# Performance work log

Measured on AMD Instinct MI355X. Metric: run time of the kernel, lower is better.

Reference implementation:

```python
import jax, jax.numpy as jnp
import numpy as np

# bitsandbytes NF4 codebook (16 levels, normalized to [-1, 1])
NF4_CODE = jnp.array([
    -1.0, -0.6961928009986877, -0.5250730514526367, -0.39491748809814453,
    -0.28444138169288635, -0.18477343022823334, -0.09105003625154495, 0.0,
    0.07958029955625534, 0.16093020141124725, 0.24611230194568634,
    0.33791524171829224, 0.44070982933044434, 0.5626170039176941,
    0.7229568362236023, 1.0], dtype=jnp.float32)

BLOCK = 64  # bitsandbytes default quantization blocksize
TOK, DIN, DOUT, RANK = 8192, 4096, 4096, 16
LORA_ALPHA = 16
SCALING = LORA_ALPHA / RANK ** 0.5  # rslora


def setup_inputs() -> dict:
    key = jax.random.key(0)
    k1, k2, k3, k4, k5, k6 = jax.random.split(key, 6)
    x = jax.random.normal(k1, (TOK, DIN), dtype=jnp.float32)
    w_codes = jax.random.randint(k2, (DOUT, DIN), 0, 16, dtype=jnp.int32)
    absmax = jax.random.uniform(k3, (DOUT, DIN // BLOCK), dtype=jnp.float32)
    bias = jax.random.normal(k4, (DOUT,), dtype=jnp.float32)
    lora_A = jax.random.normal(k5, (DIN, RANK), dtype=jnp.float32) * (1.0 / DIN ** 0.5)
    lora_B = jax.random.normal(k6, (RANK, DOUT), dtype=jnp.float32) * 0.02
    return {"x": x, "w_codes": w_codes, "absmax": absmax, "bias": bias,
            "lora_A": lora_A, "lora_B": lora_B}


def reference(x, w_codes, absmax, bias, lora_A, lora_B):
    # Dequantize NF4 base weight: codebook lookup * per-block absmax scale
    # W: [DOUT, DIN], absmax broadcast over blocks of 64 along DIN
    W = NF4_CODE[w_codes] * jnp.repeat(absmax, BLOCK, axis=1)
    base_out = x @ W.T + bias                      # [TOK, DOUT]
    lora_out = (x @ lora_A) @ lora_B               # low-rank path [TOK, DOUT]
    return base_out + lora_out * SCALING
```

## Files before the change

### kernel.cpp

```cpp
#include <hip/hip_runtime.h>
#include <hip/hip_bf16.h>
#include <cstdint>
#include <cstddef>

#define TOK   8192
#define DIN   4096
#define DOUT  4096
#define RANK  16
#define KE    4160
#define NKT64 (KE / 64)

#define BM 256
#define BN 256

#define PXB 512
#define DQB 8192
#define TLB 16

typedef __attribute__((ext_vector_type(8))) short bf16x8;
typedef __attribute__((ext_vector_type(4))) float f32x4;
typedef __attribute__((ext_vector_type(8))) unsigned short u16x8;

__device__ __constant__ float NF4_CODE_D[16] = {
    -1.0f, -0.6961928009986877f, -0.5250730514526367f, -0.39491748809814453f,
    -0.28444138169288635f, -0.18477343022823334f, -0.09105003625154495f, 0.0f,
    0.07958029955625534f, 0.16093020141124725f, 0.24611230194568634f,
    0.33791524171829224f, 0.44070982933044434f, 0.5626170039176941f,
    0.7229568362236023f, 1.0f};

__device__ __forceinline__ unsigned short f2bf(float f) {
    union { float f; unsigned u; } v; v.f = f;
    unsigned u = v.u;
    unsigned r = (u + 0x7FFFu + ((u >> 16) & 1u)) >> 16;
    return (unsigned short)r;
}

__device__ __forceinline__ void async_copy16(const void* g, void* l) {
    __builtin_amdgcn_global_load_lds(
        (const __attribute__((address_space(1))) void*)g,
        (__attribute__((address_space(3))) void*)l,
        16, 0, 0);
}

__global__ __launch_bounds__(256) void prep_fused(
        const float* __restrict__ x, const float* __restrict__ lora_A,
        const int* __restrict__ codes, const float* __restrict__ absmax,
        const float* __restrict__ bias, const float* __restrict__ lora_B,
        unsigned short* __restrict__ xe, unsigned short* __restrict__ we) {
    __shared__ float tab[16];
    const int bid = blockIdx.x;
    const int tid = threadIdx.x;

    if (bid < PXB) {
        const int l = tid & 63;
        const int w = tid >> 6;
        const int t0 = bid * 16 + w * 4;

        float p[4][16];
#pragma unroll
        for (int a = 0; a < 4; ++a)
#pragma unroll
            for (int r = 0; r < 16; ++r) p[a][r] = 0.f;

        for (int it = 0; it < 16; ++it) {
            const int kb = it * 256 + l * 4;
            float4 xv[4];
#pragma unroll
            for (int a = 0; a < 4; ++a)
                xv[a] = *(const float4*)(x + (size_t)(t0 + a) * DIN + kb);
#pragma unroll
            for (int a = 0; a < 4; ++a) {
                ushort4 s;
                s.x = f2bf(xv[a].x); s.y = f2bf(xv[a].y);
                s.z = f2bf(xv[a].z); s.w = f2bf(xv[a].w);
                *(ushort4*)(xe + (size_t)(t0 + a) * KE + kb) = s;
            }
#pragma unroll
            for (int j = 0; j < 4; ++j) {
                const float4* ap = (const float4*)(lora_A + (size_t)(kb + j) * RANK);
                const float4 a0 = ap[0], a1 = ap[1], a2 = ap[2], a3 = ap[3];
                const float av[16] = {a0.x, a0.y, a0.z, a0.w, a1.x, a1.y, a1.z, a1.w,
                                      a2.x, a2.y, a2.z, a2.w, a3.x, a3.y, a3.z, a3.w};
#pragma unroll
                for (int a = 0; a < 4; ++a) {
                    const float xs = (j == 0) ? xv[a].x : (j == 1) ? xv[a].y
                                    : (j == 2) ? xv[a].z : xv[a].w;
#pragma unroll
                    for (int r = 0; r < 16; ++r) p[a][r] += xs * av[r];
                }
            }
        }

#pragma unroll
        for (int a = 0; a < 4; ++a) {
#pragma unroll
            for (int r = 0; r < 16; ++r) {
                float v = p[a][r];
#pragma unroll
                for (int off = 32; off > 0; off >>= 1) v += __shfl_xor(v, off, 64);
                if (l == r)
                    xe[(size_t)(t0 + a) * KE + DIN + r] = f2bf(4.0f * v);
            }
            if (l >= 16)
                xe[(size_t)(t0 + a) * KE + DIN + l] =
                    (l == 16) ? (unsigned short)0x3F80u : (unsigned short)0u;
        }
    } else if (bid < PXB + DQB) {
        if (tid < 16) tab[tid] = NF4_CODE_D[tid];
        __syncthreads();
        const size_t t = (size_t)(bid - PXB) * 256 + tid;
        const size_t base = t * 8;
        const int o = (int)(base >> 12);
        const int k = (int)(base & (DIN - 1));
        const float am = absmax[base >> 6];
        const int4 c0 = *(const int4*)(codes + base);
        const int4 c1 = *(const int4*)(codes + base + 4);
        u16x8 ov;
        ov[0] = f2bf(tab[c0.x] * am);
        ov[1] = f2bf(tab[c0.y] * am);
        ov[2] = f2bf(tab[c0.z] * am);
        ov[3] = f2bf(tab[c0.w] * am);
        ov[4] = f2bf(tab[c1.x] * am);
        ov[5] = f2bf(tab[c1.y] * am);
        ov[6] = f2bf(tab[c1.z] * am);
        ov[7] = f2bf(tab[c1.w] * am);
        *(u16x8*)(we + (size_t)o * KE + k) = ov;
    } else {
        const int o = (bid - PXB - DQB) * 256 + tid;
        unsigned short* dst = we + (size_t)o * KE + DIN;
#pragma unroll
        for (int r = 0; r < RANK; ++r) dst[r] = f2bf(lora_B[(size_t)r * DOUT + o]);
        dst[16] = f2bf(bias[o]);
#pragma unroll
        for (int r = 17; r < 64; ++r) dst[r] = 0;
    }
}

__global__ __launch_bounds__(512, 2) void gemm_bt(const unsigned short* __restrict__ A,
                                                  const unsigned short* __restrict__ B,
                                                  float* __restrict__ C) {
    __shared__ __attribute__((aligned(1024))) char smem[4 * 32768];

    const int tid = threadIdx.x;
    const int l = tid & 63;
    const int w = tid >> 6;
    const int wm = w >> 2;
    const int wn = w & 3;

    const int tm = blockIdx.x >> 4;
    const int tn = blockIdx.x & 15;
    const int rowBase = tm * BM;
    const int colBase = tn * BN;

    int srow[2], scolb[2], loffs[2];
#pragma unroll
    for (int g = 0; g < 2; ++g) {
        const int loff = g * 8192 + tid * 16;
        const int soff = loff ^ (((loff >> 7) & 7) << 4);
        loffs[g] = loff;
        srow[g] = soff >> 6;
        scolb[g] = soff & 63;
    }

    auto stageA = [&](int tt, int kh, int slot) {
        char* dst = smem + slot * 32768;
        const int k0 = tt * 64 + kh * 32;
#pragma unroll
        for (int g = 0; g < 2; ++g)
            async_copy16((const char*)A + ((size_t)(rowBase + srow[g]) * KE + k0) * 2 + scolb[g],
                         dst + loffs[g]);
    };
    auto stageB = [&](int tt, int kh, int slot) {
        char* dst = smem + slot * 32768 + 16384;
        const int k0 = tt * 64 + kh * 32;
#pragma unroll
        for (int g = 0; g < 2; ++g)
            async_copy16((const char*)B + ((size_t)(colBase + srow[g]) * KE + k0) * 2 + scolb[g],
                         dst + loffs[g]);
    };

    const int lmask = ((l >> 1) & 7) << 4;
    const int aoff = (((wm * 128 + (l & 15)) * 64) + ((l >> 4) * 16)) ^ lmask;
    const int boff = (((wn * 64 + (l & 15)) * 64) + ((l >> 4) * 16)) ^ lmask;

    f32x4 acc[8][4];
#pragma unroll
    for (int m = 0; m < 8; ++m)
#pragma unroll
        for (int n = 0; n < 4; ++n) acc[m][n] = (f32x4){0.f, 0.f, 0.f, 0.f};

    bf16x8 aLo[4], aHi[4], aLo2[4], aHi2[4], bCur[4], bNxt[4];

    stageA(0, 0, 0); stageB(0, 0, 0);
    stageA(0, 1, 1); stageB(0, 1, 1);
    asm volatile("s_waitcnt vmcnt(4)" ::: "memory");
    __builtin_amdgcn_s_barrier();
    {
        const char* S0 = smem;
#pragma unroll
        for (int n = 0; n < 4; ++n)
            bCur[n] = *(const bf16x8*)(S0 + 16384 + boff + n * 1024);
#pragma unroll
        for (int m = 0; m < 4; ++m)
            aLo[m] = *(const bf16x8*)(S0 + aoff + m * 1024);
    }

    for (int t = 0; t < NKT64; ++t) {
        const char* S0 = smem + ((2 * t) & 3) * 32768;
        const char* S1 = smem + ((2 * t + 1) & 3) * 32768;
        const char* Sn = smem + ((2 * t + 2) & 3) * 32768;
        const int d0 = (2 * t + 2) & 3, d1 = (2 * t + 3) & 3;
        const bool more = (t + 1 < NKT64);

#pragma unroll
        for (int m = 0; m < 4; ++m)
            aHi[m] = *(const bf16x8*)(S0 + aoff + (4 + m) * 1024);
        if (more) { stageA(t + 1, 0, d0); stageB(t + 1, 0, d0); }
        __builtin_amdgcn_sched_barrier(0);
        __builtin_amdgcn_s_setprio(1);
#pragma unroll
        for (int m = 0; m < 4; ++m)
#pragma unroll
            for (int n = 0; n < 4; ++n)
                acc[m][n] = __builtin_amdgcn_mfma_f32_16x16x32_bf16(
                    aLo[m], bCur[n], acc[m][n], 0, 0, 0);
        __builtin_amdgcn_s_setprio(0);
        __builtin_amdgcn_sched_barrier(0);

        if (more) {
            asm volatile("s_waitcnt vmcnt(4)" ::: "memory");
        } else {
            asm volatile("s_waitcnt vmcnt(0)" ::: "memory");
        }
        __builtin_amdgcn_s_barrier();
        __builtin_amdgcn_sched_barrier(0);
#pragma unroll
        for (int n = 0; n < 4; ++n)
            bNxt[n] = *(const bf16x8*)(S1 + 16384 + boff + n * 1024);
#pragma unroll
        for (int m = 0; m < 4; ++m)
            aLo2[m] = *(const bf16x8*)(S1 + aoff + m * 1024);
        __builtin_amdgcn_sched_barrier(0);
        __builtin_amdgcn_s_setprio(1);
#pragma unroll
        for (int m = 0; m < 4; ++m)
#pragma unroll
            for (int n = 0; n < 4; ++n)
                acc[4 + m][n] = __builtin_amdgcn_mfma_f32_16x16x32_bf16(
                    aHi[m], bCur[n], acc[4 + m][n], 0, 0, 0);
        __builtin_amdgcn_s_setprio(0);
        __builtin_amdgcn_sched_barrier(0);

#pragma unroll
        for (int m = 0; m < 4; ++m)
            aHi2[m] = *(const bf16x8*)(S1 + aoff + (4 + m) * 1024);
        if (more) { stageA(t + 1, 1, d1); stageB(t + 1, 1, d1); }
        __builtin_amdgcn_sched_barrier(0);
        __builtin_amdgcn_s_setprio(1);
#pragma unroll
        for (int m = 0; m < 4; ++m)
#pragma unroll
            for (int n = 0; n < 4; ++n)
                acc[m][n] = __builtin_amdgcn_mfma_f32_16x16x32_bf16(
                    aLo2[m], bNxt[n], acc[m][n], 0, 0, 0);
        __builtin_amdgcn_s_setprio(0);
        __builtin_amdgcn_sched_barrier(0);

        if (more) {
            asm volatile("s_waitcnt vmcnt(4)" ::: "memory");
            __builtin_amdgcn_s_barrier();
            __builtin_amdgcn_sched_barrier(0);
#pragma unroll
            for (int n = 0; n < 4; ++n)
                bCur[n] = *(const bf16x8*)(Sn + 16384 + boff + n * 1024);
#pragma unroll
            for (int m = 0; m < 4; ++m)
                aLo[m] = *(const bf16x8*)(Sn + aoff + m * 1024);
        }
        __builtin_amdgcn_sched_barrier(0);
        __builtin_amdgcn_s_setprio(1);
#pragma unroll
        for (int m = 0; m < 4; ++m)
#pragma unroll
            for (int n = 0; n < 4; ++n)
                acc[4 + m][n] = __builtin_amdgcn_mfma_f32_16x16x32_bf16(
                    aHi2[m], bNxt[n], acc[4 + m][n], 0, 0, 0);
        __builtin_amdgcn_s_setprio(0);
        __builtin_amdgcn_sched_barrier(0);
    }

#pragma unroll
    for (int m = 0; m < 8; ++m) {
        const int rowg = rowBase + wm * 128 + m * 16 + (l >> 4) * 4;
#pragma unroll
        for (int n = 0; n < 4; ++n) {
            const int colg = colBase + wn * 64 + n * 16 + (l & 15);
            float* cp = C + (size_t)rowg * DOUT + colg;
#pragma unroll
            for (int r = 0; r < 4; ++r) cp[(size_t)r * DOUT] = acc[m][n][r];
        }
    }
}

extern "C" void kernel_launch(void* const* d_in, const int* in_sizes, int n_in,
                              void* d_out, int out_size, void* d_ws, size_t ws_size,
                              hipStream_t stream) {
    const float* x      = (const float*)d_in[0];
    const int*   codes  = (const int*)d_in[1];
    const float* absmax = (const float*)d_in[2];
    const float* bias   = (const float*)d_in[3];
    const float* lora_A = (const float*)d_in[4];
    const float* lora_B = (const float*)d_in[5];
    float* out = (float*)d_out;

    unsigned short* xe = (unsigned short*)d_ws;
    unsigned short* we = xe + (size_t)TOK * KE;

    prep_fused<<<PXB + DQB + TLB, 256, 0, stream>>>(x, lora_A, codes, absmax,
                                                    bias, lora_B, xe, we);
    gemm_bt<<<(TOK / BM) * (DOUT / BN), 512, 0, stream>>>(xe, we, out);
}
```

Baseline: 356.0 us.

## Switch GEMM to 32x32x16 MFMA, swizzle block order, and interleave A/B staging

Replaces the 16x16x32 bf16 MFMA tiles with 32x32x16 MFMA tiles. This changes the per-wave fragment layout, the LDS read offsets and the output store mapping. It also remaps blockIdx with a swizzle so that consecutive blocks share tiles for better L2 reuse. The A and B async loads are split and spread across phases, with the vmcnt waits adjusted to match. The larger MFMA shape reduces LDS fragment reads per FLOP, at the cost of a more complex schedule and a risk of mis-tuned wait counts.

```diff
diff --git a/kernel.cpp b/kernel.cpp
--- a/kernel.cpp
+++ b/kernel.cpp
@@ -18,7 +18,7 @@
 #define TLB 16
 
 typedef __attribute__((ext_vector_type(8))) short bf16x8;
-typedef __attribute__((ext_vector_type(4))) float f32x4;
+typedef __attribute__((ext_vector_type(16))) float f32x16;
 typedef __attribute__((ext_vector_type(8))) unsigned short u16x8;
 
 __device__ __constant__ float NF4_CODE_D[16] = {
@@ -147,8 +147,9 @@
     const int wm = w >> 2;
     const int wn = w & 3;
 
-    const int tm = blockIdx.x >> 4;
-    const int tn = blockIdx.x & 15;
+    const int swz = (blockIdx.x & 7) * 64 + (blockIdx.x >> 3);
+    const int tm = swz >> 4;
+    const int tn = swz & 15;
     const int rowBase = tm * BM;
     const int colBase = tn * BN;
 
@@ -179,15 +180,28 @@
                          dst + loffs[g]);
     };
 
+    const int r32 = l & 31;
+    const int h32 = (l >> 5) & 1;
     const int lmask = ((l >> 1) & 7) << 4;
-    const int aoff = (((wm * 128 + (l & 15)) * 64) + ((l >> 4) * 16)) ^ lmask;
-    const int boff = (((wn * 64 + (l & 15)) * 64) + ((l >> 4) * 16)) ^ lmask;
-
-    f32x4 acc[8][4];
-#pragma unroll
-    for (int m = 0; m < 8; ++m)
-#pragma unroll
-        for (int n = 0; n < 4; ++n) acc[m][n] = (f32x4){0.f, 0.f, 0.f, 0.f};
+    int aoffs[4][2], boffs[2][2];
+#pragma unroll
+    for (int mt = 0; mt < 4; ++mt)
+#pragma unroll
+        for (int kk = 0; kk < 2; ++kk)
+            aoffs[mt][kk] = (((wm * 128 + mt * 32 + r32) * 64) + kk * 32 + h32 * 16) ^ lmask;
+#pragma unroll
+    for (int nt = 0; nt < 2; ++nt)
+#pragma unroll
+        for (int kk = 0; kk < 2; ++kk)
+            boffs[nt][kk] = 16384 + ((((wn * 64 + nt * 32 + r32) * 64) + kk * 32 + h32 * 16) ^ lmask);
+
+    f32x16 acc[4][2];
+#pragma unroll
+    for (int mt = 0; mt < 4; ++mt)
+#pragma unroll
+        for (int nt = 0; nt < 2; ++nt)
+#pragma unroll
+            for (int r = 0; r < 16; ++r) acc[mt][nt][r] = 0.f;
 
     bf16x8 aLo[4], aHi[4], aLo2[4], aHi2[4], bCur[4], bNxt[4];
 
@@ -198,11 +212,15 @@
     {
         const char* S0 = smem;
 #pragma unroll
-        for (int n = 0; n < 4; ++n)
-            bCur[n] = *(const bf16x8*)(S0 + 16384 + boff + n * 1024);
-#pragma unroll
-        for (int m = 0; m < 4; ++m)
-            aLo[m] = *(const bf16x8*)(S0 + aoff + m * 1024);
+        for (int nt = 0; nt < 2; ++nt)
+#pragma unroll
+            for (int kk = 0; kk < 2; ++kk)
+                bCur[nt * 2 + kk] = *(const bf16x8*)(S0 + boffs[nt][kk]);
+#pragma unroll
+        for (int mt = 0; mt < 2; ++mt)
+#pragma unroll
+            for (int kk = 0; kk < 2; ++kk)
+                aLo[mt * 2 + kk] = *(const bf16x8*)(S0 + aoffs[mt][kk]);
     }
 
     for (int t = 0; t < NKT64; ++t) {
@@ -213,91 +231,115 @@
         const bool more = (t + 1 < NKT64);
 
 #pragma unroll
-        for (int m = 0; m < 4; ++m)
-            aHi[m] = *(const bf16x8*)(S0 + aoff + (4 + m) * 1024);
-        if (more) { stageA(t + 1, 0, d0); stageB(t + 1, 0, d0); }
+        for (int mt = 0; mt < 2; ++mt)
+#pragma unroll
+            for (int kk = 0; kk < 2; ++kk)
+                aHi[mt * 2 + kk] = *(const bf16x8*)(S0 + aoffs[2 + mt][kk]);
+        if (more) stageA(t + 1, 0, d0);
         __builtin_amdgcn_sched_barrier(0);
         __builtin_amdgcn_s_setprio(1);
 #pragma unroll
-        for (int m = 0; m < 4; ++m)
-#pragma unroll
-            for (int n = 0; n < 4; ++n)
-                acc[m][n] = __builtin_amdgcn_mfma_f32_16x16x32_bf16(
-                    aLo[m], bCur[n], acc[m][n], 0, 0, 0);
+        for (int kk = 0; kk < 2; ++kk)
+#pragma unroll
+            for (int mt = 0; mt < 2; ++mt)
+#pragma unroll
+                for (int nt = 0; nt < 2; ++nt)
+                    acc[mt][nt] = __builtin_amdgcn_mfma_f32_32x32x16_bf16(
+                        aLo[mt * 2 + kk], bCur[nt * 2 + kk], acc[mt][nt], 0, 0, 0);
         __builtin_amdgcn_s_setprio(0);
         __builtin_amdgcn_sched_barrier(0);
 
         if (more) {
-            asm volatile("s_waitcnt vmcnt(4)" ::: "memory");
+            asm volatile("s_waitcnt vmcnt(2)" ::: "memory");
         } else {
             asm volatile("s_waitcnt vmcnt(0)" ::: "memory");
         }
         __builtin_amdgcn_s_barrier();
         __builtin_amdgcn_sched_barrier(0);
 #pragma unroll
-        for (int n = 0; n < 4; ++n)
-            bNxt[n] = *(const bf16x8*)(S1 + 16384 + boff + n * 1024);
-#pragma unroll
-        for (int m = 0; m < 4; ++m)
-            aLo2[m] = *(const bf16x8*)(S1 + aoff + m * 1024);
+        for (int nt = 0; nt < 2; ++nt)
+#pragma unroll
+            for (int kk = 0; kk < 2; ++kk)
+                bNxt[nt * 2 + kk] = *(const bf16x8*)(S1 + boffs[nt][kk]);
+#pragma unroll
+        for (int mt = 0; mt < 2; ++mt)
+#pragma unroll
+            for (int kk = 0; kk < 2; ++kk)
+                aLo2[mt * 2 + kk] = *(const bf16x8*)(S1 + aoffs[mt][kk]);
+        if (more) stageB(t + 1, 0, d0);
         __builtin_amdgcn_sched_barrier(0);
         __builtin_amdgcn_s_setprio(1);
 #pragma unroll
-        for (int m = 0; m < 4; ++m)
-#pragma unroll
-            for (int n = 0; n < 4; ++n)
-                acc[4 + m][n] = __builtin_amdgcn_mfma_f32_16x16x32_bf16(
-                    aHi[m], bCur[n], acc[4 + m][n], 0, 0, 0);
+        for (int kk = 0; kk < 2; ++kk)
+#pragma unroll
+            for (int mt = 0; mt < 2; ++mt)
+#pragma unroll
+                for (int nt = 0; nt < 2; ++nt)
+                    acc[2 + mt][nt] = __builtin_amdgcn_mfma_f32_32x32x16_bf16(
+                        aHi[mt * 2 + kk], bCur[nt * 2 + kk], acc[2 + mt][nt], 0, 0, 0);
         __builtin_amdgcn_s_setprio(0);
         __builtin_amdgcn_sched_barrier(0);
 
 #pragma unroll
-        for (int m = 0; m < 4; ++m)
-            aHi2[m] = *(const bf16x8*)(S1 + aoff + (4 + m) * 1024);
-        if (more) { stageA(t + 1, 1, d1); stageB(t + 1, 1, d1); }
+        for (int mt = 0; mt < 2; ++mt)
+#pragma unroll
+            for (int kk = 0; kk < 2; ++kk)
+                aHi2[mt * 2 + kk] = *(const bf16x8*)(S1 + aoffs[2 + mt][kk]);
+        if (more) stageA(t + 1, 1, d1);
         __builtin_amdgcn_sched_barrier(0);
         __builtin_amdgcn_s_setprio(1);
 #pragma unroll
-        for (int m = 0; m < 4; ++m)
-#pragma unroll
-            for (int n = 0; n < 4; ++n)
-                acc[m][n] = __builtin_amdgcn_mfma_f32_16x16x32_bf16(
-                    aLo2[m], bNxt[n], acc[m][n], 0, 0, 0);
+        for (int kk = 0; kk < 2; ++kk)
+#pragma unroll
+            for (int mt = 0; mt < 2; ++mt)
+#pragma unroll
+                for (int nt = 0; nt < 2; ++nt)
+                    acc[mt][nt] = __builtin_amdgcn_mfma_f32_32x32x16_bf16(
+                        aLo2[mt * 2 + kk], bNxt[nt * 2 + kk], acc[mt][nt], 0, 0, 0);
         __builtin_amdgcn_s_setprio(0);
         __builtin_amdgcn_sched_barrier(0);
 
         if (more) {
-            asm volatile("s_waitcnt vmcnt(4)" ::: "memory");
+            asm volatile("s_waitcnt vmcnt(2)" ::: "memory");
             __builtin_amdgcn_s_barrier();
             __builtin_amdgcn_sched_barrier(0);
 #pragma unroll
-            for (int n = 0; n < 4; ++n)
-                bCur[n] = *(const bf16x8*)(Sn + 16384 + boff + n * 1024);
-#pragma unroll
-            for (int m = 0; m < 4; ++m)
-                aLo[m] = *(const bf16x8*)(Sn + aoff + m * 1024);
+            for (int nt = 0; nt < 2; ++nt)
+#pragma unroll
+                for (int kk = 0; kk < 2; ++kk)
+                    bCur[nt * 2 + kk] = *(const bf16x8*)(Sn + boffs[nt][kk]);
+#pragma unroll
+            for (int mt = 0; mt < 2; ++mt)
+#pragma unroll
+                for (int kk = 0; kk < 2; ++kk)
+                    aLo[mt * 2 + kk] = *(const bf16x8*)(Sn + aoffs[mt][kk]);
+            stageB(t + 1, 1, d1);
         }
         __builtin_amdgcn_sched_barrier(0);
         __builtin_amdgcn_s_setprio(1);
 #pragma unroll
-        for (int m = 0; m < 4; ++m)
-#pragma unroll
-            for (int n = 0; n < 4; ++n)
-                acc[4 + m][n] = __builtin_amdgcn_mfma_f32_16x16x32_bf16(
-                    aHi2[m], bNxt[n], acc[4 + m][n], 0, 0, 0);
+        for (int kk = 0; kk < 2; ++kk)
+#pragma unroll
+            for (int mt = 0; mt < 2; ++mt)
+#pragma unroll
+                for (int nt = 0; nt < 2; ++nt)
+                    acc[2 + mt][nt] = __builtin_amdgcn_mfma_f32_32x32x16_bf16(
+                        aHi2[mt * 2 + kk], bNxt[nt * 2 + kk], acc[2 + mt][nt], 0, 0, 0);
         __builtin_amdgcn_s_setprio(0);
         __builtin_amdgcn_sched_barrier(0);
     }
 
 #pragma unroll
-    for (int m = 0; m < 8; ++m) {
-        const int rowg = rowBase + wm * 128 + m * 16 + (l >> 4) * 4;
-#pragma unroll
-        for (int n = 0; n < 4; ++n) {
-            const int colg = colBase + wn * 64 + n * 16 + (l & 15);
-            float* cp = C + (size_t)rowg * DOUT + colg;
-#pragma unroll
-            for (int r = 0; r < 4; ++r) cp[(size_t)r * DOUT] = acc[m][n][r];
+    for (int mt = 0; mt < 4; ++mt) {
+#pragma unroll
+        for (int nt = 0; nt < 2; ++nt) {
+            const int colg = colBase + wn * 64 + nt * 32 + r32;
+            const int rbase = rowBase + wm * 128 + mt * 32 + 4 * h32;
+#pragma unroll
+            for (int reg = 0; reg < 16; ++reg) {
+                const int rowg = rbase + (reg & 3) + 8 * (reg >> 2);
+                C[(size_t)rowg * DOUT + colg] = acc[mt][nt][reg];
+            }
         }
     }
 }
```

New measurement: 389.4 us. 9.4% more time.

## Split A/B staging across GEMM phases and widen prep-kernel x loads

Applied to the files above, without the earlier changes.

Inside the GEMM main loop, B-tile staging is moved out of the A-staging slots and issued later, after the LDS reads of the following half-step. The vmcnt waits are tightened from 4 to 2 to match. This spreads global-load issue across the MFMA phases to reduce contention and stalls. Separately, the prep kernel now processes 8 x values per lane per iteration with 16-byte bf16 stores instead of 4 with 8-byte stores, halving loop iterations. The risks are wrong vmcnt accounting and B loads landing closer to their consumers.

```diff
diff --git a/kernel.cpp b/kernel.cpp
--- a/kernel.cpp
+++ b/kernel.cpp
@@ -62,29 +62,38 @@
 #pragma unroll
             for (int r = 0; r < 16; ++r) p[a][r] = 0.f;
 
-        for (int it = 0; it < 16; ++it) {
-            const int kb = it * 256 + l * 4;
-            float4 xv[4];
-#pragma unroll
-            for (int a = 0; a < 4; ++a)
-                xv[a] = *(const float4*)(x + (size_t)(t0 + a) * DIN + kb);
+        for (int it = 0; it < 8; ++it) {
+            const int kb = it * 512 + l * 8;
+            float4 xv[4][2];
 #pragma unroll
             for (int a = 0; a < 4; ++a) {
-                ushort4 s;
-                s.x = f2bf(xv[a].x); s.y = f2bf(xv[a].y);
-                s.z = f2bf(xv[a].z); s.w = f2bf(xv[a].w);
-                *(ushort4*)(xe + (size_t)(t0 + a) * KE + kb) = s;
+                const float* xp = x + (size_t)(t0 + a) * DIN + kb;
+                xv[a][0] = *(const float4*)(xp);
+                xv[a][1] = *(const float4*)(xp + 4);
             }
 #pragma unroll
-            for (int j = 0; j < 4; ++j) {
+            for (int a = 0; a < 4; ++a) {
+                u16x8 s;
+#pragma unroll
+                for (int h = 0; h < 2; ++h) {
+                    s[h * 4 + 0] = f2bf(xv[a][h].x);
+                    s[h * 4 + 1] = f2bf(xv[a][h].y);
+                    s[h * 4 + 2] = f2bf(xv[a][h].z);
+                    s[h * 4 + 3] = f2bf(xv[a][h].w);
+                }
+                *(u16x8*)(xe + (size_t)(t0 + a) * KE + kb) = s;
+            }
+#pragma unroll
+            for (int j = 0; j < 8; ++j) {
                 const float4* ap = (const float4*)(lora_A + (size_t)(kb + j) * RANK);
                 const float4 a0 = ap[0], a1 = ap[1], a2 = ap[2], a3 = ap[3];
                 const float av[16] = {a0.x, a0.y, a0.z, a0.w, a1.x, a1.y, a1.z, a1.w,
                                       a2.x, a2.y, a2.z, a2.w, a3.x, a3.y, a3.z, a3.w};
 #pragma unroll
                 for (int a = 0; a < 4; ++a) {
-                    const float xs = (j == 0) ? xv[a].x : (j == 1) ? xv[a].y
-                                    : (j == 2) ? xv[a].z : xv[a].w;
+                    const float4 xh = xv[a][j >> 2];
+                    const float xs = (j & 3) == 0 ? xh.x : (j & 3) == 1 ? xh.y
+                                   : (j & 3) == 2 ? xh.z : xh.w;
 #pragma unroll
                     for (int r = 0; r < 16; ++r) p[a][r] += xs * av[r];
                 }
@@ -215,7 +224,7 @@
 #pragma unroll
         for (int m = 0; m < 4; ++m)
             aHi[m] = *(const bf16x8*)(S0 + aoff + (4 + m) * 1024);
-        if (more) { stageA(t + 1, 0, d0); stageB(t + 1, 0, d0); }
+        if (more) stageA(t + 1, 0, d0);
         __builtin_amdgcn_sched_barrier(0);
         __builtin_amdgcn_s_setprio(1);
 #pragma unroll
@@ -228,7 +237,7 @@
         __builtin_amdgcn_sched_barrier(0);
 
         if (more) {
-            asm volatile("s_waitcnt vmcnt(4)" ::: "memory");
+            asm volatile("s_waitcnt vmcnt(2)" ::: "memory");
         } else {
             asm volatile("s_waitcnt vmcnt(0)" ::: "memory");
         }
@@ -240,6 +249,7 @@
 #pragma unroll
         for (int m = 0; m < 4; ++m)
             aLo2[m] = *(const bf16x8*)(S1 + aoff + m * 1024);
+        if (more) stageB(t + 1, 0, d0);
         __builtin_amdgcn_sched_barrier(0);
         __builtin_amdgcn_s_setprio(1);
 #pragma unroll
@@ -254,7 +264,7 @@
 #pragma unroll
         for (int m = 0; m < 4; ++m)
             aHi2[m] = *(const bf16x8*)(S1 + aoff + (4 + m) * 1024);
-        if (more) { stageA(t + 1, 1, d1); stageB(t + 1, 1, d1); }
+        if (more) stageA(t + 1, 1, d1);
         __builtin_amdgcn_sched_barrier(0);
         __builtin_amdgcn_s_setprio(1);
 #pragma unroll
@@ -267,7 +277,7 @@
         __builtin_amdgcn_sched_barrier(0);
 
         if (more) {
-            asm volatile("s_waitcnt vmcnt(4)" ::: "memory");
+            asm volatile("s_waitcnt vmcnt(2)" ::: "memory");
             __builtin_amdgcn_s_barrier();
             __builtin_amdgcn_sched_barrier(0);
 #pragma unroll
@@ -276,6 +286,7 @@
 #pragma unroll
             for (int m = 0; m < 4; ++m)
                 aLo[m] = *(const bf16x8*)(Sn + aoff + m * 1024);
+            stageB(t + 1, 1, d1);
         }
         __builtin_amdgcn_sched_barrier(0);
         __builtin_amdgcn_s_setprio(1);
```

Result: slower. 363.1 us (+2.0%).
